# Optimization experiments

Measured on AMD Instinct MI355X. Metric: run time of the kernel, lower is better.

## Reference

```python
import jax, jax.numpy as jnp
import numpy as np

T, B, D, H = 2048, 32, 512, 512  # seq_len, batch, input_size, hidden_size


def setup_inputs() -> dict:
    key = jax.random.key(0)
    k1, k2, k3, k4, k5 = jax.random.split(key, 5)
    s = 1.0 / np.sqrt(H)  # torch LSTMCell init scale (uniform); we use scaled normal
    return {
        "inputs": jax.random.normal(k1, (T, B, D), dtype=jnp.float32),
        "W_ih": jax.random.normal(k2, (4 * H, D), dtype=jnp.float32) * s,
        "W_hh": jax.random.normal(k3, (4 * H, H), dtype=jnp.float32) * s,
        "b_ih": jax.random.normal(k4, (4 * H,), dtype=jnp.float32) * s,
        "b_hh": jax.random.normal(k5, (4 * H,), dtype=jnp.float32) * s,
    }


def reference(inputs, W_ih, W_hh, b_ih, b_hh):
    """TimeRecurrentCell(lstm=True, batch_first=False, reverse=False) wrapping an LSTMCell.

    inputs: [T, B, D]. Returns (outputs [T, B, H], (h_T, c_T)).
    PyTorch gate order in the fused weight: i, f, g, o.
    """
    batch = inputs.shape[1]
    h0 = jnp.zeros((batch, H), dtype=inputs.dtype)
    c0 = jnp.zeros((batch, H), dtype=inputs.dtype)
    # Precompute input projections for all timesteps in one big GEMM: [T, B, 4H]
    x_proj = jnp.einsum('tbd,gd->tbg', inputs, W_ih) + b_ih + b_hh

    def step(carry, xg_t):
        h, c = carry
        gates = xg_t + h @ W_hh.T  # [B, 4H]
        i, f, g, o = jnp.split(gates, 4, axis=-1)
        i = jax.nn.sigmoid(i)
        f = jax.nn.sigmoid(f)
        g = jnp.tanh(g)
        o = jax.nn.sigmoid(o)
        c_new = f * c + i * g
        h_new = o * jnp.tanh(c_new)
        return (h_new, c_new), h_new

    (h_T, c_T), outputs = jax.lax.scan(step, (h0, c0), x_proj)
    return outputs, (h_T, c_T)
```

## Files before the change

### kernel.cpp

```cpp
#include <hip/hip_runtime.h>

#define T_STEPS 2048
#define BATCH   32
#define DIM     512
#define HID     512
#define NB      256
#define JB      2
#define NTHR    512
#define NKS     8
#define WSTRIDE   516
#define WSTRIDE_F 1028
#define HSTRIDE 36
#define MROWS   (T_STEPS * BATCH)
#define NCOLS   (4 * HID)

#define HBUF_BYTES (2 * HID * BATCH * 4)
#define BARR_BYTES 4096
#define XP_BYTES   ((size_t)MROWS * NCOLS * 2)

#define FMA4(A, W, P) do { A.x = fmaf(W.x, P.x, A.x); A.y = fmaf(W.y, P.y, A.y); \
                           A.z = fmaf(W.z, P.z, A.z); A.w = fmaf(W.w, P.w, A.w); } while (0)
#define FMAS(A, s, P) do { A.x = fmaf(s, P.x, A.x); A.y = fmaf(s, P.y, A.y); \
                           A.z = fmaf(s, P.z, A.z); A.w = fmaf(s, P.w, A.w); } while (0)

#define LLC_LOAD4(dst, p) \
    asm volatile("global_load_dwordx4 %0, %1, off sc0 sc1" : "=v"(dst) : "v"(p) : "memory")

__device__ __forceinline__ float hsum4(float4 a) { return (a.x + a.y) + (a.z + a.w); }

__device__ __forceinline__ unsigned short f2b(float f) {
    unsigned u = __float_as_uint(f);
    return (unsigned short)((u + 0x7fffu + ((u >> 16) & 1u)) >> 16);
}

using s8v = __attribute__((ext_vector_type(8))) short;
using f4v = __attribute__((ext_vector_type(4))) float;

__global__ __launch_bounds__(256, 2) void xproj_gemm(
    const float* __restrict__ x, const float* __restrict__ Wih,
    unsigned short* __restrict__ xp)
{
    __shared__ unsigned short As[64][40];
    __shared__ unsigned short Bs[64][40];
    const int tid  = threadIdx.x;
    const int mi   = blockIdx.x >> 5;
    const int ni   = blockIdx.x & 31;
    const int lane = tid & 63;
    const int wv   = tid >> 6;
    const int wr   = (wv >> 1) * 32, wc = (wv & 1) * 32;
    const int r0   = lane & 15, kb = (lane >> 4) * 8;

    f4v acc00 = {0,0,0,0}, acc01 = {0,0,0,0}, acc10 = {0,0,0,0}, acc11 = {0,0,0,0};

    for (int ko = 0; ko < 512; ko += 32) {
        __syncthreads();
#pragma unroll
        for (int i = tid; i < 512; i += 256) {
            int row = i >> 3, kq = i & 7;
            float4 va = *(const float4*)(x   + (size_t)(mi * 64 + row) * 512 + ko + kq * 4);
            float4 vb = *(const float4*)(Wih + (size_t)(ni * 64 + row) * 512 + ko + kq * 4);
            uint2 ua = make_uint2((unsigned)f2b(va.x) | ((unsigned)f2b(va.y) << 16),
                                  (unsigned)f2b(va.z) | ((unsigned)f2b(va.w) << 16));
            uint2 ub = make_uint2((unsigned)f2b(vb.x) | ((unsigned)f2b(vb.y) << 16),
                                  (unsigned)f2b(vb.z) | ((unsigned)f2b(vb.w) << 16));
            *(uint2*)&As[row][kq * 4] = ua;
            *(uint2*)&Bs[row][kq * 4] = ub;
        }
        __syncthreads();
        s8v a0 = *(const s8v*)&As[wr      + r0][kb];
        s8v a1 = *(const s8v*)&As[wr + 16 + r0][kb];
        s8v b0 = *(const s8v*)&Bs[wc      + r0][kb];
        s8v b1 = *(const s8v*)&Bs[wc + 16 + r0][kb];
        acc00 = __builtin_amdgcn_mfma_f32_16x16x32_bf16(a0, b0, acc00, 0, 0, 0);
        acc01 = __builtin_amdgcn_mfma_f32_16x16x32_bf16(a0, b1, acc01, 0, 0, 0);
        acc10 = __builtin_amdgcn_mfma_f32_16x16x32_bf16(a1, b0, acc10, 0, 0, 0);
        acc11 = __builtin_amdgcn_mfma_f32_16x16x32_bf16(a1, b1, acc11, 0, 0, 0);
    }
    const int rb = (lane >> 4) * 4, cb = lane & 15;
#pragma unroll
    for (int j = 0; j < 4; ++j) {
        size_t rA = (size_t)(mi * 64 + wr + rb + j) * NCOLS + (ni * 64 + wc + cb);
        size_t rB = (size_t)(mi * 64 + wr + 16 + rb + j) * NCOLS + (ni * 64 + wc + cb);
        xp[rA]        = f2b(acc00[j]);
        xp[rA + 16]   = f2b(acc01[j]);
        xp[rB]        = f2b(acc10[j]);
        xp[rB + 16]   = f2b(acc11[j]);
    }
}

__global__ __launch_bounds__(NTHR, 1) void lstm_persist_xp(
    const unsigned short* __restrict__ xp,
    const float* __restrict__ Whh,
    const float* __restrict__ bih, const float* __restrict__ bhh,
    float* __restrict__ out,
    float* hbuf, int* barr)
{
    __shared__ float Wl[8][WSTRIDE];
    __shared__ float hl[HID][HSTRIDE];
    __shared__ float part[NKS][8][33];
    __shared__ float bias[8];
    __shared__ float cst[JB * BATCH];

    const int tid = threadIdx.x;
    const int bj  = blockIdx.x;
    const int r   = tid & 7;
    const int bg  = (tid >> 3) & 7;
    const int ks  = tid >> 6;
    const int bg4 = bg * 4;

    for (int i = tid; i < 8 * 128; i += NTHR) {
        int row = i >> 7, q = i & 127;
        int R = ((row >> 1) << 9) + (bj << 1) + (row & 1);
        *(float4*)&Wl[row][q * 4] = ((const float4*)(Whh + (size_t)R * HID))[q];
    }
    if (tid < 8) {
        int R = ((tid >> 1) << 9) + (bj << 1) + (tid & 1);
        bias[tid] = bih[R] + bhh[R];
    }
    if (tid < JB * BATCH) cst[tid] = 0.f;
    __syncthreads();

    int* garr = barr;
    const int jj = tid & 1, bb = tid >> 1;
    const size_t xbase0 = (size_t)bb * NCOLS + (bj << 1) + jj;

    for (int t = 0; t < T_STEPS; ++t) {
        unsigned short u0 = 0, u1 = 0, u2 = 0, u3 = 0;
        if (tid < 64) {
            const unsigned short* p = xp + (size_t)t * BATCH * NCOLS + xbase0;
            u0 = p[0]; u1 = p[512]; u2 = p[1024]; u3 = p[1536];
        }

        if (tid < 64) {
            const int target = t * 32;
            const int* cp = &garr[(tid & 7) * 32];
            while (true) {
                int v = __hip_atomic_load(cp, __ATOMIC_RELAXED, __HIP_MEMORY_SCOPE_AGENT);
                if (__all(v >= target)) break;
                __builtin_amdgcn_s_sleep(1);
            }
        }
        __syncthreads();

        {
            const float* hsrc = hbuf + (size_t)(t & 1) * (HID * BATCH) + (tid << 2);
            float* wp = &hl[tid >> 3][(tid & 7) << 2];
            float4 vv[8];
#pragma unroll
            for (int it = 0; it < 8; ++it) {
                int p = (it + bj) & 7;
                LLC_LOAD4(vv[it], hsrc + p * 2048);
            }
            asm volatile("s_waitcnt vmcnt(0)" ::: "memory");
            __builtin_amdgcn_sched_barrier(0);
#pragma unroll
            for (int it = 0; it < 8; ++it) {
                int p = (it + bj) & 7;
                *(float4*)(wp + p * 64 * HSTRIDE) = vv[it];
            }
        }
        __syncthreads();

        float4 H = {0, 0, 0, 0};
#pragma unroll 4
        for (int kq = 0; kq < 16; ++kq) {
            int K = (ks << 6) + (kq << 2);
            float4 w4 = *(const float4*)&Wl[r][K];
            float4 h0 = *(const float4*)&hl[K + 0][bg4];
            float4 h1 = *(const float4*)&hl[K + 1][bg4];
            float4 h2 = *(const float4*)&hl[K + 2][bg4];
            float4 h3 = *(const float4*)&hl[K + 3][bg4];
            FMAS(H, w4.x, h0); FMAS(H, w4.y, h1); FMAS(H, w4.z, h2); FMAS(H, w4.w, h3);
        }
        part[ks][r][bg4 + 0] = H.x;
        part[ks][r][bg4 + 1] = H.y;
        part[ks][r][bg4 + 2] = H.z;
        part[ks][r][bg4 + 3] = H.w;
        __syncthreads();

        float hval = 0.f, cval = 0.f;
        if (tid < 64) {
            float gi = bias[0 + jj] + __uint_as_float((unsigned)u0 << 16);
            float gf = bias[2 + jj] + __uint_as_float((unsigned)u1 << 16);
            float gg = bias[4 + jj] + __uint_as_float((unsigned)u2 << 16);
            float go = bias[6 + jj] + __uint_as_float((unsigned)u3 << 16);
#pragma unroll
            for (int kk = 0; kk < NKS; ++kk) {
                gi += part[kk][0 + jj][bb];
                gf += part[kk][2 + jj][bb];
                gg += part[kk][4 + jj][bb];
                go += part[kk][6 + jj][bb];
            }
            float ig = 1.f / (1.f + __expf(-gi));
            float fg = 1.f / (1.f + __expf(-gf));
            float g  = tanhf(gg);
            float og = 1.f / (1.f + __expf(-go));
            float c  = fg * cst[tid] + ig * g;
            cst[tid] = c;
            float h  = og * tanhf(c);
            hval = h; cval = c;
            int j = (bj << 1) + jj;
            __hip_atomic_store(hbuf + (size_t)((t + 1) & 1) * (HID * BATCH) + (size_t)j * BATCH + bb,
                               h, __ATOMIC_RELAXED, __HIP_MEMORY_SCOPE_AGENT);
        }

        asm volatile("s_waitcnt vmcnt(0)" ::: "memory");
        if (tid == 0) {
            __hip_atomic_fetch_add(&garr[(bj & 7) * 32], 1, __ATOMIC_RELAXED,
                                   __HIP_MEMORY_SCOPE_AGENT);
        }

        if (tid < 64) {
            int j = (bj << 1) + jj;
            out[((size_t)t * BATCH + bb) * HID + j] = hval;
            if (t == T_STEPS - 1) {
                out[(size_t)T_STEPS * BATCH * HID + (size_t)bb * HID + j] = hval;
                out[(size_t)T_STEPS * BATCH * HID + (size_t)BATCH * HID + (size_t)bb * HID + j] = cval;
            }
        }
    }
}

__global__ __launch_bounds__(NTHR, 1) void lstm_persist_full(
    const float* __restrict__ x, const float* __restrict__ Wih,
    const float* __restrict__ Whh,
    const float* __restrict__ bih, const float* __restrict__ bhh,
    float* __restrict__ out, float* hbuf, int* barr)
{
    __shared__ float Wl[8][WSTRIDE_F];
    __shared__ float hl[HID][HSTRIDE];
    __shared__ float part[NKS][8][33];
    __shared__ float bias[8];
    __shared__ float cst[JB * BATCH];

    const int tid = threadIdx.x;
    const int bj  = blockIdx.x;
    const int r   = tid & 7;
    const int bg  = (tid >> 3) & 7;
    const int ks  = tid >> 6;
    const int bg4 = bg * 4;
    const int k0  = ks * 16;

    for (int i = tid; i < 8 * 256; i += NTHR) {
        int row = i >> 8, q = i & 255;
        int R = ((row >> 1) << 9) + (bj << 1) + (row & 1);
        float4 v = (q < 128) ? ((const float4*)(Wih + (size_t)R * DIM))[q]
                             : ((const float4*)(Whh + (size_t)R * HID))[q - 128];
        *(float4*)&Wl[row][q * 4] = v;
    }
    if (tid < 8) {
        int R = ((tid >> 1) << 9) + (bj << 1) + (tid & 1);
        bias[tid] = bih[R] + bhh[R];
    }
    if (tid < JB * BATCH) cst[tid] = 0.f;
    __syncthreads();

    const float4* __restrict__ wrow = (const float4*)&Wl[r][0];
    int* garr = barr;
    int* gctr = barr + 8 * 32;
    int* rel  = barr + 8 * 32 + 32;

    for (int t = 0; t < T_STEPS; ++t) {
        float4 A0 = {0,0,0,0}, A1 = {0,0,0,0}, A2 = {0,0,0,0}, A3 = {0,0,0,0};
        {
            const float* xb = x + ((size_t)t * BATCH + bg4) * DIM;
            const float4* v0 = (const float4*)xb;
            const float4* v1 = (const float4*)(xb + DIM);
            const float4* v2 = (const float4*)(xb + 2 * DIM);
            const float4* v3 = (const float4*)(xb + 3 * DIM);
#pragma unroll 4
            for (int k = 0; k < 16; ++k) {
                float4 w = wrow[k0 + k];
                float4 p0 = v0[k0 + k], p1 = v1[k0 + k], p2 = v2[k0 + k], p3 = v3[k0 + k];
                FMA4(A0, w, p0); FMA4(A1, w, p1); FMA4(A2, w, p2); FMA4(A3, w, p3);
            }
        }
        if (tid == 0) {
            while (__hip_atomic_load(rel, __ATOMIC_RELAXED, __HIP_MEMORY_SCOPE_AGENT) < t)
                __builtin_amdgcn_s_sleep(1);
        }
        __syncthreads();
        {
            const float* hsrc = hbuf + (size_t)(t & 1) * (HID * BATCH) + (tid << 2);
            float4 v0, v1, v2, v3, v4, v5, v6, v7;
            LLC_LOAD4(v0, hsrc);
            LLC_LOAD4(v1, hsrc + 2048);
            LLC_LOAD4(v2, hsrc + 4096);
            LLC_LOAD4(v3, hsrc + 6144);
            LLC_LOAD4(v4, hsrc + 8192);
            LLC_LOAD4(v5, hsrc + 10240);
            LLC_LOAD4(v6, hsrc + 12288);
            LLC_LOAD4(v7, hsrc + 14336);
            asm volatile("s_waitcnt vmcnt(0)" ::: "memory");
            __builtin_amdgcn_sched_barrier(0);
            float* wp = &hl[tid >> 3][(tid & 7) << 2];
            *(float4*)(wp + 0 * 64 * HSTRIDE) = v0;
            *(float4*)(wp + 1 * 64 * HSTRIDE) = v1;
            *(float4*)(wp + 2 * 64 * HSTRIDE) = v2;
            *(float4*)(wp + 3 * 64 * HSTRIDE) = v3;
            *(float4*)(wp + 4 * 64 * HSTRIDE) = v4;
            *(float4*)(wp + 5 * 64 * HSTRIDE) = v5;
            *(float4*)(wp + 6 * 64 * HSTRIDE) = v6;
            *(float4*)(wp + 7 * 64 * HSTRIDE) = v7;
        }
        __syncthreads();
        float4 H = {0,0,0,0};
#pragma unroll 4
        for (int kq = 0; kq < 16; ++kq) {
            int K = (ks << 6) + (kq << 2);
            float4 w4 = *(const float4*)&Wl[r][512 + K];
            float4 h0 = *(const float4*)&hl[K + 0][bg4];
            float4 h1 = *(const float4*)&hl[K + 1][bg4];
            float4 h2 = *(const float4*)&hl[K + 2][bg4];
            float4 h3 = *(const float4*)&hl[K + 3][bg4];
            FMAS(H, w4.x, h0); FMAS(H, w4.y, h1); FMAS(H, w4.z, h2); FMAS(H, w4.w, h3);
        }
        part[ks][r][bg4 + 0] = hsum4(A0) + H.x;
        part[ks][r][bg4 + 1] = hsum4(A1) + H.y;
        part[ks][r][bg4 + 2] = hsum4(A2) + H.z;
        part[ks][r][bg4 + 3] = hsum4(A3) + H.w;
        __syncthreads();
        float hval = 0.f, cval = 0.f;
        if (tid < JB * BATCH) {
            int jj = tid & 1, b = tid >> 1;
            float gi = bias[0 + jj], gf = bias[2 + jj], gg = bias[4 + jj], go = bias[6 + jj];
#pragma unroll
            for (int kk = 0; kk < NKS; ++kk) {
                gi += part[kk][0 + jj][b];
                gf += part[kk][2 + jj][b];
                gg += part[kk][4 + jj][b];
                go += part[kk][6 + jj][b];
            }
            float ig = 1.f / (1.f + __expf(-gi));
            float fg = 1.f / (1.f + __expf(-gf));
            float g  = tanhf(gg);
            float og = 1.f / (1.f + __expf(-go));
            float c  = fg * cst[tid] + ig * g;
            cst[tid] = c;
            float h  = og * tanhf(c);
            hval = h; cval = c;
            int j = (bj << 1) + jj;
            __hip_atomic_store(hbuf + (size_t)((t + 1) & 1) * (HID * BATCH) + (size_t)j * BATCH + b,
                               h, __ATOMIC_RELAXED, __HIP_MEMORY_SCOPE_AGENT);
        }
        asm volatile("s_waitcnt vmcnt(0)" ::: "memory");
        if (tid == 0) {
            int grp = bj & 7;
            int old = __hip_atomic_fetch_add(&garr[grp * 32], 1, __ATOMIC_RELAXED,
                                             __HIP_MEMORY_SCOPE_AGENT);
            if (old == (t + 1) * 32 - 1) {
                int o2 = __hip_atomic_fetch_add(gctr, 1, __ATOMIC_RELAXED,
                                                __HIP_MEMORY_SCOPE_AGENT);
                if (o2 == (t + 1) * 8 - 1) {
                    __hip_atomic_fetch_add(rel, 1, __ATOMIC_RELAXED,
                                           __HIP_MEMORY_SCOPE_AGENT);
                }
            }
        }
        if (tid < JB * BATCH) {
            int jj = tid & 1, b = tid >> 1;
            int j = (bj << 1) + jj;
            out[((size_t)t * BATCH + b) * HID + j] = hval;
            if (t == T_STEPS - 1) {
                out[(size_t)T_STEPS * BATCH * HID + (size_t)b * HID + j] = hval;
                out[(size_t)T_STEPS * BATCH * HID + (size_t)BATCH * HID + (size_t)b * HID + j] = cval;
            }
        }
    }
}

extern "C" void kernel_launch(void* const* d_in, const int* in_sizes, int n_in,
                              void* d_out, int out_size, void* d_ws, size_t ws_size,
                              hipStream_t stream) {
    (void)in_sizes; (void)n_in; (void)out_size;
    const float* x   = (const float*)d_in[0];
    const float* Wih = (const float*)d_in[1];
    const float* Whh = (const float*)d_in[2];
    const float* bih = (const float*)d_in[3];
    const float* bhh = (const float*)d_in[4];
    float* outp = (float*)d_out;
    float* hbuf = (float*)d_ws;
    int*   barr = (int*)((char*)d_ws + HBUF_BYTES);

    hipMemsetAsync(d_ws, 0, HBUF_BYTES + BARR_BYTES, stream);

    const size_t need = (size_t)HBUF_BYTES + BARR_BYTES + XP_BYTES;
    if (ws_size >= need) {
        unsigned short* xp = (unsigned short*)((char*)d_ws + HBUF_BYTES + BARR_BYTES);
        xproj_gemm<<<(MROWS / 64) * (NCOLS / 64), 256, 0, stream>>>(x, Wih, xp);
        lstm_persist_xp<<<NB, NTHR, 0, stream>>>(xp, Whh, bih, bhh, outp, hbuf, barr);
    } else {
        lstm_persist_full<<<NB, NTHR, 0, stream>>>(x, Wih, Whh, bih, bhh, outp, hbuf, barr);
    }
}
```

Measured before the change: 9.485 ms.

## Keep W_hh slice in registers and reduce LSTM partial sums with DPP

The persistent LSTM kernel now keeps each thread's 8x8 slice of W_hh in registers and loads its h values straight from global memory into registers, dropping the LDS staging of both. Partial dot products are reduced across neighbouring lanes with DPP adds before a smaller LDS exchange. This removes two block-wide barriers and most LDS traffic from every step of the serial recurrence. Bias and cell state move into registers, and the inter-block barrier counters are spread over 32 slots instead of 8, with every wave polling them itself. The cost is much higher register use per thread and more polling traffic on the barrier counters.

```diff
diff --git a/kernel.cpp b/kernel.cpp
--- a/kernel.cpp
+++ b/kernel.cpp
@@ -8,7 +8,6 @@
 #define JB      2
 #define NTHR    512
 #define NKS     8
-#define WSTRIDE   516
 #define WSTRIDE_F 1028
 #define HSTRIDE 36
 #define MROWS   (T_STEPS * BATCH)
@@ -25,6 +24,9 @@
 
 #define LLC_LOAD4(dst, p) \
     asm volatile("global_load_dwordx4 %0, %1, off sc0 sc1" : "=v"(dst) : "v"(p) : "memory")
+
+#define DPPADD(v, ctrl) \
+    ((v) + __int_as_float(__builtin_amdgcn_update_dpp(0, __float_as_int(v), ctrl, 0xf, 0xf, true)))
 
 __device__ __forceinline__ float hsum4(float4 a) { return (a.x + a.y) + (a.z + a.w); }
 
@@ -95,33 +97,34 @@
     float* __restrict__ out,
     float* hbuf, int* barr)
 {
-    __shared__ float Wl[8][WSTRIDE];
-    __shared__ float hl[HID][HSTRIDE];
-    __shared__ float part[NKS][8][33];
-    __shared__ float bias[8];
-    __shared__ float cst[JB * BATCH];
+    __shared__ float part[8][2][8][36];
 
     const int tid = threadIdx.x;
     const int bj  = blockIdx.x;
-    const int r   = tid & 7;
-    const int bg  = (tid >> 3) & 7;
-    const int ks  = tid >> 6;
-    const int bg4 = bg * 4;
-
-    for (int i = tid; i < 8 * 128; i += NTHR) {
-        int row = i >> 7, q = i & 127;
+    const int kss = tid & 7;
+    const int bg4 = ((tid >> 3) & 7) << 2;
+    const int wv  = tid >> 6;
+    const int K0  = wv * 64 + kss * 8;
+    const int jj  = tid & 1, bb = tid >> 1;
+
+    float wregs[64];
+#pragma unroll
+    for (int row = 0; row < 8; ++row) {
         int R = ((row >> 1) << 9) + (bj << 1) + (row & 1);
-        *(float4*)&Wl[row][q * 4] = ((const float4*)(Whh + (size_t)R * HID))[q];
-    }
-    if (tid < 8) {
-        int R = ((tid >> 1) << 9) + (bj << 1) + (tid & 1);
-        bias[tid] = bih[R] + bhh[R];
-    }
-    if (tid < JB * BATCH) cst[tid] = 0.f;
-    __syncthreads();
-
+        float4 a = *(const float4*)(Whh + (size_t)R * HID + K0);
+        float4 b = *(const float4*)(Whh + (size_t)R * HID + K0 + 4);
+        wregs[row*8+0]=a.x; wregs[row*8+1]=a.y; wregs[row*8+2]=a.z; wregs[row*8+3]=a.w;
+        wregs[row*8+4]=b.x; wregs[row*8+5]=b.y; wregs[row*8+6]=b.z; wregs[row*8+7]=b.w;
+    }
+    float bi0 = 0, bi1 = 0, bi2 = 0, bi3 = 0, creg = 0.f;
+    if (tid < 64) {
+        int cj = (bj << 1) + jj;
+        bi0 = bih[cj]        + bhh[cj];
+        bi1 = bih[512 + cj]  + bhh[512 + cj];
+        bi2 = bih[1024 + cj] + bhh[1024 + cj];
+        bi3 = bih[1536 + cj] + bhh[1536 + cj];
+    }
     int* garr = barr;
-    const int jj = tid & 1, bb = tid >> 1;
     const size_t xbase0 = (size_t)bb * NCOLS + (bj << 1) + jj;
 
     for (int t = 0; t < T_STEPS; ++t) {
@@ -131,72 +134,72 @@
             u0 = p[0]; u1 = p[512]; u2 = p[1024]; u3 = p[1536];
         }
 
-        if (tid < 64) {
-            const int target = t * 32;
-            const int* cp = &garr[(tid & 7) * 32];
+        {
+            const int target = t * 8;
+            const int* cp = &garr[(tid & 31) * 32];
             while (true) {
                 int v = __hip_atomic_load(cp, __ATOMIC_RELAXED, __HIP_MEMORY_SCOPE_AGENT);
                 if (__all(v >= target)) break;
                 __builtin_amdgcn_s_sleep(1);
             }
         }
-        __syncthreads();
-
+
+        float4 hv[8];
         {
-            const float* hsrc = hbuf + (size_t)(t & 1) * (HID * BATCH) + (tid << 2);
-            float* wp = &hl[tid >> 3][(tid & 7) << 2];
-            float4 vv[8];
-#pragma unroll
-            for (int it = 0; it < 8; ++it) {
-                int p = (it + bj) & 7;
-                LLC_LOAD4(vv[it], hsrc + p * 2048);
-            }
+            const float* hsrc = hbuf + (size_t)(t & 1) * (HID * BATCH) + (size_t)K0 * BATCH + bg4;
+#pragma unroll
+            for (int kk = 0; kk < 8; ++kk) LLC_LOAD4(hv[kk], hsrc + kk * BATCH);
             asm volatile("s_waitcnt vmcnt(0)" ::: "memory");
             __builtin_amdgcn_sched_barrier(0);
-#pragma unroll
-            for (int it = 0; it < 8; ++it) {
-                int p = (it + bj) & 7;
-                *(float4*)(wp + p * 64 * HSTRIDE) = vv[it];
-            }
-        }
-        __syncthreads();
-
-        float4 H = {0, 0, 0, 0};
-#pragma unroll 4
-        for (int kq = 0; kq < 16; ++kq) {
-            int K = (ks << 6) + (kq << 2);
-            float4 w4 = *(const float4*)&Wl[r][K];
-            float4 h0 = *(const float4*)&hl[K + 0][bg4];
-            float4 h1 = *(const float4*)&hl[K + 1][bg4];
-            float4 h2 = *(const float4*)&hl[K + 2][bg4];
-            float4 h3 = *(const float4*)&hl[K + 3][bg4];
-            FMAS(H, w4.x, h0); FMAS(H, w4.y, h1); FMAS(H, w4.z, h2); FMAS(H, w4.w, h3);
-        }
-        part[ks][r][bg4 + 0] = H.x;
-        part[ks][r][bg4 + 1] = H.y;
-        part[ks][r][bg4 + 2] = H.z;
-        part[ks][r][bg4 + 3] = H.w;
+        }
+
+        float4 acc[8];
+#pragma unroll
+        for (int row = 0; row < 8; ++row) acc[row] = make_float4(0.f, 0.f, 0.f, 0.f);
+#pragma unroll
+        for (int kk = 0; kk < 8; ++kk) {
+#pragma unroll
+            for (int row = 0; row < 8; ++row)
+                FMAS(acc[row], wregs[row*8+kk], hv[kk]);
+        }
+
+#pragma unroll
+        for (int row = 0; row < 8; ++row) {
+            acc[row].x = DPPADD(acc[row].x, 0xB1); acc[row].y = DPPADD(acc[row].y, 0xB1);
+            acc[row].z = DPPADD(acc[row].z, 0xB1); acc[row].w = DPPADD(acc[row].w, 0xB1);
+            acc[row].x = DPPADD(acc[row].x, 0x4E); acc[row].y = DPPADD(acc[row].y, 0x4E);
+            acc[row].z = DPPADD(acc[row].z, 0x4E); acc[row].w = DPPADD(acc[row].w, 0x4E);
+        }
+        if ((kss & 3) == 0) {
+            int k2 = kss >> 2;
+#pragma unroll
+            for (int row = 0; row < 8; ++row)
+                *(float4*)&part[wv][k2][row][bg4] = acc[row];
+        }
         __syncthreads();
 
         float hval = 0.f, cval = 0.f;
         if (tid < 64) {
-            float gi = bias[0 + jj] + __uint_as_float((unsigned)u0 << 16);
-            float gf = bias[2 + jj] + __uint_as_float((unsigned)u1 << 16);
-            float gg = bias[4 + jj] + __uint_as_float((unsigned)u2 << 16);
-            float go = bias[6 + jj] + __uint_as_float((unsigned)u3 << 16);
-#pragma unroll
-            for (int kk = 0; kk < NKS; ++kk) {
-                gi += part[kk][0 + jj][bb];
-                gf += part[kk][2 + jj][bb];
-                gg += part[kk][4 + jj][bb];
-                go += part[kk][6 + jj][bb];
+            float gi = bi0 + __uint_as_float((unsigned)u0 << 16);
+            float gf = bi1 + __uint_as_float((unsigned)u1 << 16);
+            float gg = bi2 + __uint_as_float((unsigned)u2 << 16);
+            float go = bi3 + __uint_as_float((unsigned)u3 << 16);
+#pragma unroll
+            for (int w = 0; w < 8; ++w) {
+#pragma unroll
+                for (int k2 = 0; k2 < 2; ++k2) {
+                    gi += part[w][k2][0 + jj][bb];
+                    gf += part[w][k2][2 + jj][bb];
+                    gg += part[w][k2][4 + jj][bb];
+                    go += part[w][k2][6 + jj][bb];
+                }
             }
             float ig = 1.f / (1.f + __expf(-gi));
             float fg = 1.f / (1.f + __expf(-gf));
             float g  = tanhf(gg);
             float og = 1.f / (1.f + __expf(-go));
-            float c  = fg * cst[tid] + ig * g;
-            cst[tid] = c;
+            float c  = fg * creg + ig * g;
+            creg = c;
             float h  = og * tanhf(c);
             hval = h; cval = c;
             int j = (bj << 1) + jj;
@@ -206,7 +209,7 @@
 
         asm volatile("s_waitcnt vmcnt(0)" ::: "memory");
         if (tid == 0) {
-            __hip_atomic_fetch_add(&garr[(bj & 7) * 32], 1, __ATOMIC_RELAXED,
+            __hip_atomic_fetch_add(&garr[(bj & 31) * 32], 1, __ATOMIC_RELAXED,
                                    __HIP_MEMORY_SCOPE_AGENT);
         }
 
```

Result: slower. 14.10 ms (+48.7%).
